# Performance work log

Measured on AMD Instinct MI355X. Metric: run time of the kernel, lower is better.

The kernel has to match this reference:

```python
import jax, jax.numpy as jnp
import numpy as np

B, L, A, D = 16, 256, 128, 4   # batch, seq_len, n_agents, per-agent feat (enc_in//n_agents)
H = 64                          # d_model / TGCN hidden
DFF = 256                       # decoder d_ff
PRED, COUT = 64, 8              # pred_len, c_out
EPS = 1e-6
SELF_W = 1.0 / EPS              # self-loop weight: 1/(0 + 1e-6)


def setup_inputs() -> dict:
    key = jax.random.key(0)
    ks = jax.random.split(key, 20)
    g = lambda i, shape, s=1.0: jax.random.normal(ks[i], shape, jnp.float32) * s
    z = lambda shape: jnp.zeros(shape, jnp.float32)
    return {
        "x": g(0, (B, L, A * D)),
        "x_mark_enc": g(1, (B, L, 4)),
        "x_dec": g(2, (B, PRED, A * D)),
        "x_mark_dec": g(3, (B, PRED, 4)),
        # GCNConv weights/biases for z, r, h gates (stored [in, out])
        "W_z": g(4, (D, H), 0.3), "b_z": z((H,)),
        "W_r": g(5, (D, H), 0.3), "b_r": z((H,)),
        "W_h": g(6, (D, H), 0.3), "b_h": z((H,)),
        # TGCN gate linears: Linear(2H, H), stored [2H, H]
        "Lz_w": g(7, (2 * H, H), 0.1), "Lz_b": z((H,)),
        "Lr_w": g(8, (2 * H, H), 0.1), "Lr_b": z((H,)),
        "Lh_w": g(9, (2 * H, H), 0.1), "Lh_b": z((H,)),
        # decoder: Linear(H, DFF) -> ReLU -> Linear(DFF, PRED*COUT)
        "D1_w": g(10, (H, DFF), 0.1), "D1_b": z((DFF,)),
        "D2_w": g(11, (DFF, PRED * COUT), 0.05), "D2_b": z((PRED * COUT,)),
    }


def _gcn(xr, a_hat, w, b):
    # GCNConv: A_hat @ (X @ W) + b, batched over (b, t)
    xw = jnp.einsum('blad,dh->blah', xr, w)
    return jnp.einsum('blae,bleh->blah', a_hat, xw) + b


def _forward(x, W_z, b_z, W_r, b_r, W_h, b_h, Lz_w, Lz_b, Lr_w, Lr_b,
             Lh_w, Lh_b, D1_w, D1_b, D2_w, D2_b):
    xr = x.reshape(B, L, A, D)
    # dense all-pairs adjacency: w_ij = 1/(||x_i-x_j|| + 1e-6); diag kept at 1e6
    sq = jnp.sum(xr * xr, axis=-1)                               # [B,L,A]
    d2 = sq[..., :, None] + sq[..., None, :] - 2.0 * jnp.einsum('blad,bled->blae', xr, xr)
    d2 = jnp.maximum(d2, 0.0)
    eye = jnp.eye(A, dtype=bool)
    dist = jnp.sqrt(jnp.where(eye, 1.0, d2))                     # safe sqrt on diag
    w = jnp.where(eye, SELF_W, 1.0 / (dist + EPS))               # [B,L,A,A]
    # symmetric GCN normalization: D^{-1/2} W D^{-1/2}
    dinv = 1.0 / jnp.sqrt(jnp.sum(w, axis=-1))                   # [B,L,A]
    a_hat = dinv[..., :, None] * w * dinv[..., None, :]
    # TGCN GRU cell with H0 = 0 (hidden state is never carried in the loop)
    cz = _gcn(xr, a_hat, W_z, b_z)
    cr = _gcn(xr, a_hat, W_r, b_r)
    ch = _gcn(xr, a_hat, W_h, b_h)
    zeros = jnp.zeros_like(cz)
    Z = jax.nn.sigmoid(jnp.concatenate([cz, zeros], -1) @ Lz_w + Lz_b)
    R = jax.nn.sigmoid(jnp.concatenate([cr, zeros], -1) @ Lr_w + Lr_b)
    Ht = jnp.tanh(jnp.concatenate([ch, zeros * R], -1) @ Lh_w + Lh_b)
    Hs = (1.0 - Z) * Ht                                          # Z*H0 + (1-Z)*Ht, H0=0
    h = jax.nn.relu(Hs)                                          # [B,L,A,H]
    pooled = h.mean(axis=2).mean(axis=1)                         # agent pool, then seq pool -> [B,H]
    y = jax.nn.relu(pooled @ D1_w + D1_b) @ D2_w + D2_b          # decoder (dropout=eval identity)
    return y.reshape(B, PRED, COUT)


def reference(x, x_mark_enc, x_dec, x_mark_dec, W_z, b_z, W_r, b_r, W_h, b_h,
              Lz_w, Lz_b, Lr_w, Lr_b, Lh_w, Lh_b, D1_w, D1_b, D2_w, D2_b):
    # x_mark_enc / x_dec / x_mark_dec are accepted but unused, as in the torch forward
    return _forward(x, W_z, b_z, W_r, b_r, W_h, b_h, Lz_w, Lz_b, Lr_w, Lr_b,
                    Lh_w, Lh_b, D1_w, D1_b, D2_w, D2_b)
```

## Files before the change

### kernel.cpp

```cpp
#include <hip/hip_runtime.h>
#include <hip/hip_bf16.h>
#include <math.h>

#define B_ 16
#define L_ 256
#define A_ 128
#define D_ 4
#define H_ 64
#define DFF_ 256
#define PRED_ 64
#define COUT_ 8

#define WS_GW   0
#define WS_GB   512
#define WS_PART 640

#define L2E 1.4426950408889634f

typedef float v2 __attribute__((ext_vector_type(2)));

__global__ __launch_bounds__(256) void precomp_kernel(
    const float* __restrict__ W_z, const float* __restrict__ b_z,
    const float* __restrict__ W_h, const float* __restrict__ b_h,
    const float* __restrict__ Lz_w, const float* __restrict__ Lz_b,
    const float* __restrict__ Lh_w, const float* __restrict__ Lh_b,
    float* __restrict__ ws)
{
    int t = threadIdx.x;
    for (int idx = t; idx < 512; idx += 256) {
        int g = idx >> 8;
        int d = (idx >> 6) & 3;
        int j = idx & 63;
        const float* W  = g ? W_h  : W_z;
        const float* Lw = g ? Lh_w : Lz_w;
        float acc = 0.f;
        for (int h = 0; h < 64; ++h)
            acc += W[d * 64 + h] * Lw[h * 64 + j];
        ws[WS_GW + g * 256 + d * 64 + j] = acc * (g ? 2.f * L2E : L2E);
    }
    if (t < 128) {
        int g = t >> 6;
        int j = t & 63;
        const float* bg = g ? b_h  : b_z;
        const float* Lw = g ? Lh_w : Lz_w;
        const float* Lb = g ? Lh_b : Lz_b;
        float acc = Lb[j];
        for (int h = 0; h < 64; ++h)
            acc += bg[h] * Lw[h * 64 + j];
        ws[WS_GB + g * 64 + j] = acc * (g ? 2.f * L2E : L2E);
    }
}

#define REP32(M) M(0) M(1) M(2) M(3) M(4) M(5) M(6) M(7) \
                 M(8) M(9) M(10) M(11) M(12) M(13) M(14) M(15) \
                 M(16) M(17) M(18) M(19) M(20) M(21) M(22) M(23) \
                 M(24) M(25) M(26) M(27) M(28) M(29) M(30) M(31)

__global__ __launch_bounds__(512, 6) void tgcn_kernel(
    const float* __restrict__ x,
    const float* __restrict__ ws_w,
    float* __restrict__ part)
{
    __shared__ float4 xr4_s[128];
    __shared__ float4 xs4_s[128];
    __shared__ float4 M4_s[128];
    __shared__ float  gw_s[512];
    __shared__ float  gb_s[128];
    __shared__ float  red_s[8][64];

    const int t  = threadIdx.x;
    const int bl = blockIdx.x;

    if (t < 128) {
        xr4_s[t] = ((const float4*)(x + (size_t)bl * (A_ * D_)))[t];
    } else if (t < 384) {
        int i = t - 128;
        gw_s[i]       = ws_w[WS_GW + i];
        gw_s[i + 256] = ws_w[WS_GW + i + 256];
    } else {
        gb_s[t - 384] = ws_w[WS_GB + (t - 384)];
    }
    __syncthreads();

    const int r = t >> 2;
    const int q = t & 3;

    const float4 xa = xr4_s[r];
    const v2 xa01 = {xa.x, xa.y};
    const v2 xa23 = {xa.z, xa.w};

#define DECLW(i) float w##i;
    REP32(DECLW)
#undef DECLW
    float rs0 = 0.f, rs1 = 0.f;
#define PASS1(i) { \
        float4 xe = xr4_s[((i) << 2) | q]; \
        v2 d01 = xa01 - (v2){xe.x, xe.y}; \
        v2 d23 = xa23 - (v2){xe.z, xe.w}; \
        v2 s2 = d01 * d01; \
        s2 = __builtin_elementwise_fma(d23, d23, s2); \
        float d2 = s2.x + s2.y; \
        w##i = fminf(__builtin_amdgcn_rsqf(d2), 1.0e6f); \
        if ((i) & 1) rs1 += w##i; else rs0 += w##i; }
    REP32(PASS1)
#undef PASS1
    float rs = rs0 + rs1;
    rs += __shfl_xor(rs, 1);
    rs += __shfl_xor(rs, 2);
    const float dinv = __builtin_amdgcn_rsqf(rs);
    if (q == 0)
        xs4_s[r] = make_float4(dinv * xa.x, dinv * xa.y, dinv * xa.z, dinv * xa.w);
    __syncthreads();

    v2 mA = {0.f, 0.f};
    v2 mB = {0.f, 0.f};
#define PASS2(i) { \
        float4 u = xs4_s[((i) << 2) | q]; \
        v2 wv2 = {w##i, w##i}; \
        mA = __builtin_elementwise_fma(wv2, (v2){u.x, u.y}, mA); \
        mB = __builtin_elementwise_fma(wv2, (v2){u.z, u.w}, mB); }
    REP32(PASS2)
#undef PASS2
    float m0 = mA.x, m1 = mA.y, m2 = mB.x, m3 = mB.y;
    m0 += __shfl_xor(m0, 1); m0 += __shfl_xor(m0, 2);
    m1 += __shfl_xor(m1, 1); m1 += __shfl_xor(m1, 2);
    m2 += __shfl_xor(m2, 1); m2 += __shfl_xor(m2, 2);
    m3 += __shfl_xor(m3, 1); m3 += __shfl_xor(m3, 2);
    if (q == 0)
        M4_s[r] = make_float4(dinv * m0, dinv * m1, dinv * m2, dinv * m3);
    __syncthreads();

    {
        const int j  = t & 63;
        const int g  = t >> 6;
        const v2 W0 = {gw_s[j],       gw_s[256 + j]};
        const v2 W1 = {gw_s[64 + j],  gw_s[320 + j]};
        const v2 W2 = {gw_s[128 + j], gw_s[384 + j]};
        const v2 W3 = {gw_s[192 + j], gw_s[448 + j]};
        const v2 Bzh = {gb_s[j], gb_s[64 + j]};
        float acc = 0.f;
        #pragma unroll
        for (int i = 0; i < 16; ++i) {
            float4 mv = M4_s[g * 16 + i];
            v2 zh = __builtin_elementwise_fma((v2){mv.x, mv.x}, W0, Bzh);
            zh = __builtin_elementwise_fma((v2){mv.y, mv.y}, W1, zh);
            zh = __builtin_elementwise_fma((v2){mv.z, mv.z}, W2, zh);
            zh = __builtin_elementwise_fma((v2){mv.w, mv.w}, W3, zh);
            float ez = __builtin_amdgcn_exp2f(zh.x);
            float e2 = __builtin_amdgcn_exp2f(zh.y);
            float num = e2 - 1.f;
            float den = (1.f + ez) * (1.f + e2);
            float hv  = num * __builtin_amdgcn_rcpf(den);
            acc += fmaxf(hv, 0.f);
        }
        red_s[g][j] = acc;
    }
    __syncthreads();

    if (t < 64) {
        float s = red_s[0][t] + red_s[1][t] + red_s[2][t] + red_s[3][t]
                + red_s[4][t] + red_s[5][t] + red_s[6][t] + red_s[7][t];
        part[(size_t)bl * 64 + t] = s;
    }
}

__global__ __launch_bounds__(1024) void pooldec_kernel(
    const float* __restrict__ part,
    const float* __restrict__ D1_w, const float* __restrict__ D1_b,
    const float* __restrict__ D2_w, const float* __restrict__ D2_b,
    float* __restrict__ out)
{
    __shared__ float red_s[16][64];
    __shared__ float pooled_s[64];
    __shared__ float t1_s[256];
    const int t = threadIdx.x, b = blockIdx.x;

    {
        const int j = t & 63, g = t >> 6;
        const float* pb = part + ((size_t)b * L_ + g * 16) * 64;
        float s = 0.f;
        #pragma unroll
        for (int i = 0; i < 16; ++i) s += pb[i * 64 + j];
        red_s[g][j] = s;
    }
    __syncthreads();
    if (t < 64) {
        float s = 0.f;
        #pragma unroll
        for (int g = 0; g < 16; ++g) s += red_s[g][t];
        pooled_s[t] = s * (1.f / ((float)L_ * (float)A_));
    }
    __syncthreads();

    {
        const int o = t >> 2, sub = t & 3;
        float acc = 0.f;
        #pragma unroll
        for (int hh = 0; hh < 16; ++hh) {
            int h = sub * 16 + hh;
            acc += pooled_s[h] * D1_w[h * 256 + o];
        }
        acc += __shfl_xor(acc, 1);
        acc += __shfl_xor(acc, 2);
        if (sub == 0) t1_s[o] = fmaxf(acc + D1_b[o], 0.f);
    }
    __syncthreads();

    {
        const int o = t >> 1, kh = t & 1;
        float acc = 0.f;
        for (int kk = 0; kk < 128; ++kk) {
            int k = kh * 128 + kk;
            acc += t1_s[k] * D2_w[k * 512 + o];
        }
        acc += __shfl_xor(acc, 1);
        if (kh == 0) out[(size_t)b * 512 + o] = acc + D2_b[o];
    }
}

extern "C" void kernel_launch(void* const* d_in, const int* in_sizes, int n_in,
                              void* d_out, int out_size, void* d_ws, size_t ws_size,
                              hipStream_t stream)
{
    const float* x    = (const float*)d_in[0];
    const float* W_z  = (const float*)d_in[4];
    const float* b_z  = (const float*)d_in[5];
    const float* W_h  = (const float*)d_in[8];
    const float* b_h  = (const float*)d_in[9];
    const float* Lz_w = (const float*)d_in[10];
    const float* Lz_b = (const float*)d_in[11];
    const float* Lh_w = (const float*)d_in[14];
    const float* Lh_b = (const float*)d_in[15];
    const float* D1_w = (const float*)d_in[16];
    const float* D1_b = (const float*)d_in[17];
    const float* D2_w = (const float*)d_in[18];
    const float* D2_b = (const float*)d_in[19];

    float* ws  = (float*)d_ws;
    float* out = (float*)d_out;

    precomp_kernel<<<1, 256, 0, stream>>>(W_z, b_z, W_h, b_h,
                                          Lz_w, Lz_b, Lh_w, Lh_b, ws);
    tgcn_kernel<<<B_ * L_, 512, 0, stream>>>(x, ws, ws + WS_PART);
    pooldec_kernel<<<B_, 1024, 0, stream>>>(ws + WS_PART, D1_w, D1_b,
                                            D2_w, D2_b, out);
}
```

Measured before the change: 69.73 us.

## Process two agent rows per thread in TGCN kernel with 256-thread blocks

Halves the block size of the main TGCN kernel and has each thread compute adjacency weights and aggregation for two agent rows (r and r+64). Each neighbour float4 loaded from shared memory is reused for both rows, which cuts LDS traffic per FLOP, and the gate stage loops over 32 agents per group instead of 16. The trade-off is double the register arrays for the weights (64 floats) and lower thread-level parallelism per block, which may reduce occupancy or add spills.

```diff
diff --git a/kernel.cpp b/kernel.cpp
--- a/kernel.cpp
+++ b/kernel.cpp
@@ -51,12 +51,7 @@
     }
 }
 
-#define REP32(M) M(0) M(1) M(2) M(3) M(4) M(5) M(6) M(7) \
-                 M(8) M(9) M(10) M(11) M(12) M(13) M(14) M(15) \
-                 M(16) M(17) M(18) M(19) M(20) M(21) M(22) M(23) \
-                 M(24) M(25) M(26) M(27) M(28) M(29) M(30) M(31)
-
-__global__ __launch_bounds__(512, 6) void tgcn_kernel(
+__global__ __launch_bounds__(256, 4) void tgcn_kernel(
     const float* __restrict__ x,
     const float* __restrict__ ws_w,
     float* __restrict__ part)
@@ -66,68 +61,99 @@
     __shared__ float4 M4_s[128];
     __shared__ float  gw_s[512];
     __shared__ float  gb_s[128];
-    __shared__ float  red_s[8][64];
+    __shared__ float  red_s[4][64];
 
     const int t  = threadIdx.x;
     const int bl = blockIdx.x;
 
     if (t < 128) {
         xr4_s[t] = ((const float4*)(x + (size_t)bl * (A_ * D_)))[t];
-    } else if (t < 384) {
-        int i = t - 128;
-        gw_s[i]       = ws_w[WS_GW + i];
-        gw_s[i + 256] = ws_w[WS_GW + i + 256];
-    } else {
-        gb_s[t - 384] = ws_w[WS_GB + (t - 384)];
-    }
+        gb_s[t]  = ws_w[WS_GB + t];
+    }
+    gw_s[t]       = ws_w[WS_GW + t];
+    gw_s[t + 256] = ws_w[WS_GW + t + 256];
     __syncthreads();
 
     const int r = t >> 2;
     const int q = t & 3;
 
-    const float4 xa = xr4_s[r];
-    const v2 xa01 = {xa.x, xa.y};
-    const v2 xa23 = {xa.z, xa.w};
-
-#define DECLW(i) float w##i;
-    REP32(DECLW)
-#undef DECLW
-    float rs0 = 0.f, rs1 = 0.f;
-#define PASS1(i) { \
-        float4 xe = xr4_s[((i) << 2) | q]; \
-        v2 d01 = xa01 - (v2){xe.x, xe.y}; \
-        v2 d23 = xa23 - (v2){xe.z, xe.w}; \
-        v2 s2 = d01 * d01; \
-        s2 = __builtin_elementwise_fma(d23, d23, s2); \
-        float d2 = s2.x + s2.y; \
-        w##i = fminf(__builtin_amdgcn_rsqf(d2), 1.0e6f); \
-        if ((i) & 1) rs1 += w##i; else rs0 += w##i; }
-    REP32(PASS1)
-#undef PASS1
-    float rs = rs0 + rs1;
-    rs += __shfl_xor(rs, 1);
-    rs += __shfl_xor(rs, 2);
-    const float dinv = __builtin_amdgcn_rsqf(rs);
-    if (q == 0)
-        xs4_s[r] = make_float4(dinv * xa.x, dinv * xa.y, dinv * xa.z, dinv * xa.w);
-    __syncthreads();
-
-    v2 mA = {0.f, 0.f};
-    v2 mB = {0.f, 0.f};
-#define PASS2(i) { \
-        float4 u = xs4_s[((i) << 2) | q]; \
-        v2 wv2 = {w##i, w##i}; \
-        mA = __builtin_elementwise_fma(wv2, (v2){u.x, u.y}, mA); \
-        mB = __builtin_elementwise_fma(wv2, (v2){u.z, u.w}, mB); }
-    REP32(PASS2)
-#undef PASS2
-    float m0 = mA.x, m1 = mA.y, m2 = mB.x, m3 = mB.y;
-    m0 += __shfl_xor(m0, 1); m0 += __shfl_xor(m0, 2);
-    m1 += __shfl_xor(m1, 1); m1 += __shfl_xor(m1, 2);
-    m2 += __shfl_xor(m2, 1); m2 += __shfl_xor(m2, 2);
-    m3 += __shfl_xor(m3, 1); m3 += __shfl_xor(m3, 2);
-    if (q == 0)
-        M4_s[r] = make_float4(dinv * m0, dinv * m1, dinv * m2, dinv * m3);
+    const float4 xa0 = xr4_s[r];
+    const float4 xa1 = xr4_s[r + 64];
+    const v2 a0_01 = {xa0.x, xa0.y};
+    const v2 a0_23 = {xa0.z, xa0.w};
+    const v2 a1_01 = {xa1.x, xa1.y};
+    const v2 a1_23 = {xa1.z, xa1.w};
+
+    float wu[32];
+    float wv[32];
+    float rsA0 = 0.f, rsA1 = 0.f, rsB0 = 0.f, rsB1 = 0.f;
+    #pragma unroll
+    for (int k = 0; k < 32; ++k) {
+        float4 xe = xr4_s[(k << 2) | q];
+        v2 e01 = {xe.x, xe.y};
+        v2 e23 = {xe.z, xe.w};
+        v2 dA01 = a0_01 - e01;
+        v2 dA23 = a0_23 - e23;
+        v2 sA = dA01 * dA01;
+        sA = __builtin_elementwise_fma(dA23, dA23, sA);
+        float wA = fminf(__builtin_amdgcn_rsqf(sA.x + sA.y), 1.0e6f);
+        v2 dB01 = a1_01 - e01;
+        v2 dB23 = a1_23 - e23;
+        v2 sB = dB01 * dB01;
+        sB = __builtin_elementwise_fma(dB23, dB23, sB);
+        float wB = fminf(__builtin_amdgcn_rsqf(sB.x + sB.y), 1.0e6f);
+        wu[k] = wA;
+        wv[k] = wB;
+        if (k & 1) { rsA1 += wA; rsB1 += wB; }
+        else       { rsA0 += wA; rsB0 += wB; }
+    }
+    float rsA = rsA0 + rsA1;
+    float rsB = rsB0 + rsB1;
+    rsA += __shfl_xor(rsA, 1); rsA += __shfl_xor(rsA, 2);
+    rsB += __shfl_xor(rsB, 1); rsB += __shfl_xor(rsB, 2);
+    const float dinvA = __builtin_amdgcn_rsqf(rsA);
+    const float dinvB = __builtin_amdgcn_rsqf(rsB);
+    if (q == 0) {
+        xs4_s[r]      = make_float4(dinvA * xa0.x, dinvA * xa0.y,
+                                    dinvA * xa0.z, dinvA * xa0.w);
+        xs4_s[r + 64] = make_float4(dinvB * xa1.x, dinvB * xa1.y,
+                                    dinvB * xa1.z, dinvB * xa1.w);
+    }
+    __syncthreads();
+
+    v2 mA01 = {0.f, 0.f};
+    v2 mA23 = {0.f, 0.f};
+    v2 mB01 = {0.f, 0.f};
+    v2 mB23 = {0.f, 0.f};
+    #pragma unroll
+    for (int k = 0; k < 32; ++k) {
+        float4 xu = xr4_s[0];
+        xu = xs4_s[(k << 2) | q];
+        v2 u01 = {xu.x, xu.y};
+        v2 u23 = {xu.z, xu.w};
+        v2 wA2 = {wu[k], wu[k]};
+        v2 wB2 = {wv[k], wv[k]};
+        mA01 = __builtin_elementwise_fma(wA2, u01, mA01);
+        mA23 = __builtin_elementwise_fma(wA2, u23, mA23);
+        mB01 = __builtin_elementwise_fma(wB2, u01, mB01);
+        mB23 = __builtin_elementwise_fma(wB2, u23, mB23);
+    }
+    float mA0 = mA01.x, mA1 = mA01.y, mA2 = mA23.x, mA3 = mA23.y;
+    float mB0 = mB01.x, mB1 = mB01.y, mB2 = mB23.x, mB3 = mB23.y;
+    mA0 += __shfl_xor(mA0, 1); mA0 += __shfl_xor(mA0, 2);
+    mA1 += __shfl_xor(mA1, 1); mA1 += __shfl_xor(mA1, 2);
+    mA2 += __shfl_xor(mA2, 1); mA2 += __shfl_xor(mA2, 2);
+    mA3 += __shfl_xor(mA3, 1); mA3 += __shfl_xor(mA3, 2);
+    mB0 += __shfl_xor(mB0, 1); mB0 += __shfl_xor(mB0, 2);
+    mB1 += __shfl_xor(mB1, 1); mB1 += __shfl_xor(mB1, 2);
+    mB2 += __shfl_xor(mB2, 1); mB2 += __shfl_xor(mB2, 2);
+    mB3 += __shfl_xor(mB3, 1); mB3 += __shfl_xor(mB3, 2);
+    if (q == 0) {
+        M4_s[r]      = make_float4(dinvA * mA0, dinvA * mA1,
+                                   dinvA * mA2, dinvA * mA3);
+        M4_s[r + 64] = make_float4(dinvB * mB0, dinvB * mB1,
+                                   dinvB * mB2, dinvB * mB3);
+    }
     __syncthreads();
 
     {
@@ -140,8 +166,8 @@
         const v2 Bzh = {gb_s[j], gb_s[64 + j]};
         float acc = 0.f;
         #pragma unroll
-        for (int i = 0; i < 16; ++i) {
-            float4 mv = M4_s[g * 16 + i];
+        for (int i = 0; i < 32; ++i) {
+            float4 mv = M4_s[g * 32 + i];
             v2 zh = __builtin_elementwise_fma((v2){mv.x, mv.x}, W0, Bzh);
             zh = __builtin_elementwise_fma((v2){mv.y, mv.y}, W1, zh);
             zh = __builtin_elementwise_fma((v2){mv.z, mv.z}, W2, zh);
@@ -158,9 +184,8 @@
     __syncthreads();
 
     if (t < 64) {
-        float s = red_s[0][t] + red_s[1][t] + red_s[2][t] + red_s[3][t]
-                + red_s[4][t] + red_s[5][t] + red_s[6][t] + red_s[7][t];
-        part[(size_t)bl * 64 + t] = s;
+        part[(size_t)bl * 64 + t] = red_s[0][t] + red_s[1][t]
+                                  + red_s[2][t] + red_s[3][t];
     }
 }
 
@@ -241,7 +266,7 @@
 
     precomp_kernel<<<1, 256, 0, stream>>>(W_z, b_z, W_h, b_h,
                                           Lz_w, Lz_b, Lh_w, Lh_b, ws);
-    tgcn_kernel<<<B_ * L_, 512, 0, stream>>>(x, ws, ws + WS_PART);
+    tgcn_kernel<<<B_ * L_, 256, 0, stream>>>(x, ws, ws + WS_PART);
     pooldec_kernel<<<B_, 1024, 0, stream>>>(ws + WS_PART, D1_w, D1_b,
                                             D2_w, D2_b, out);
 }
```

Result: slower. 79.93 us (+14.6%).

## Recompute adjacency weights instead of caching, two rows per thread group

Applied to the files above, without the earlier changes.

The TGCN kernel no longer holds 32 adjacency weights per thread in registers. Each 8-thread group now handles two agent rows and recomputes the distance-based weights in the aggregation pass, folding the neighbour's dinv in directly, so the scaled-x shared buffer becomes a per-agent dinv array. This trades roughly double the rsqrt and distance arithmetic for lower register pressure and shared reuse of each neighbour load across two rows, and the occupancy hint drops from 6 to 4. The tiny weight-precompute kernel is also spread over 5 blocks with partial unrolling.

```diff
diff --git a/kernel.cpp b/kernel.cpp
--- a/kernel.cpp
+++ b/kernel.cpp
@@ -19,50 +19,47 @@
 
 typedef float v2 __attribute__((ext_vector_type(2)));
 
-__global__ __launch_bounds__(256) void precomp_kernel(
+__global__ __launch_bounds__(128) void precomp_kernel(
     const float* __restrict__ W_z, const float* __restrict__ b_z,
     const float* __restrict__ W_h, const float* __restrict__ b_h,
     const float* __restrict__ Lz_w, const float* __restrict__ Lz_b,
     const float* __restrict__ Lh_w, const float* __restrict__ Lh_b,
     float* __restrict__ ws)
 {
-    int t = threadIdx.x;
-    for (int idx = t; idx < 512; idx += 256) {
-        int g = idx >> 8;
-        int d = (idx >> 6) & 3;
-        int j = idx & 63;
+    const int idx = blockIdx.x * 128 + threadIdx.x;
+    if (idx < 512) {
+        const int g = idx >> 8;
+        const int d = (idx >> 6) & 3;
+        const int j = idx & 63;
         const float* W  = g ? W_h  : W_z;
         const float* Lw = g ? Lh_w : Lz_w;
         float acc = 0.f;
+        #pragma unroll 8
         for (int h = 0; h < 64; ++h)
             acc += W[d * 64 + h] * Lw[h * 64 + j];
         ws[WS_GW + g * 256 + d * 64 + j] = acc * (g ? 2.f * L2E : L2E);
-    }
-    if (t < 128) {
-        int g = t >> 6;
-        int j = t & 63;
+    } else {
+        const int i = idx - 512;
+        const int g = i >> 6;
+        const int j = i & 63;
         const float* bg = g ? b_h  : b_z;
         const float* Lw = g ? Lh_w : Lz_w;
         const float* Lb = g ? Lh_b : Lz_b;
         float acc = Lb[j];
+        #pragma unroll 8
         for (int h = 0; h < 64; ++h)
             acc += bg[h] * Lw[h * 64 + j];
         ws[WS_GB + g * 64 + j] = acc * (g ? 2.f * L2E : L2E);
     }
 }
 
-#define REP32(M) M(0) M(1) M(2) M(3) M(4) M(5) M(6) M(7) \
-                 M(8) M(9) M(10) M(11) M(12) M(13) M(14) M(15) \
-                 M(16) M(17) M(18) M(19) M(20) M(21) M(22) M(23) \
-                 M(24) M(25) M(26) M(27) M(28) M(29) M(30) M(31)
-
-__global__ __launch_bounds__(512, 6) void tgcn_kernel(
+__global__ __launch_bounds__(512, 4) void tgcn_kernel(
     const float* __restrict__ x,
     const float* __restrict__ ws_w,
     float* __restrict__ part)
 {
     __shared__ float4 xr4_s[128];
-    __shared__ float4 xs4_s[128];
+    __shared__ float  dinv_s[128];
     __shared__ float4 M4_s[128];
     __shared__ float  gw_s[512];
     __shared__ float  gb_s[128];
@@ -71,68 +68,80 @@
     const int t  = threadIdx.x;
     const int bl = blockIdx.x;
 
-    if (t < 128) {
+    if (t < 128)
         xr4_s[t] = ((const float4*)(x + (size_t)bl * (A_ * D_)))[t];
-    } else if (t < 384) {
-        int i = t - 128;
-        gw_s[i]       = ws_w[WS_GW + i];
-        gw_s[i + 256] = ws_w[WS_GW + i + 256];
-    } else {
-        gb_s[t - 384] = ws_w[WS_GB + (t - 384)];
-    }
-    __syncthreads();
-
-    const int r = t >> 2;
-    const int q = t & 3;
-
-    const float4 xa = xr4_s[r];
-    const v2 xa01 = {xa.x, xa.y};
-    const v2 xa23 = {xa.z, xa.w};
-
-#define DECLW(i) float w##i;
-    REP32(DECLW)
-#undef DECLW
-    float rs0 = 0.f, rs1 = 0.f;
-#define PASS1(i) { \
-        float4 xe = xr4_s[((i) << 2) | q]; \
-        v2 d01 = xa01 - (v2){xe.x, xe.y}; \
-        v2 d23 = xa23 - (v2){xe.z, xe.w}; \
-        v2 s2 = d01 * d01; \
-        s2 = __builtin_elementwise_fma(d23, d23, s2); \
-        float d2 = s2.x + s2.y; \
-        w##i = fminf(__builtin_amdgcn_rsqf(d2), 1.0e6f); \
-        if ((i) & 1) rs1 += w##i; else rs0 += w##i; }
-    REP32(PASS1)
-#undef PASS1
-    float rs = rs0 + rs1;
-    rs += __shfl_xor(rs, 1);
-    rs += __shfl_xor(rs, 2);
-    const float dinv = __builtin_amdgcn_rsqf(rs);
-    if (q == 0)
-        xs4_s[r] = make_float4(dinv * xa.x, dinv * xa.y, dinv * xa.z, dinv * xa.w);
-    __syncthreads();
-
-    v2 mA = {0.f, 0.f};
-    v2 mB = {0.f, 0.f};
-#define PASS2(i) { \
-        float4 u = xs4_s[((i) << 2) | q]; \
-        v2 wv2 = {w##i, w##i}; \
-        mA = __builtin_elementwise_fma(wv2, (v2){u.x, u.y}, mA); \
-        mB = __builtin_elementwise_fma(wv2, (v2){u.z, u.w}, mB); }
-    REP32(PASS2)
-#undef PASS2
-    float m0 = mA.x, m1 = mA.y, m2 = mB.x, m3 = mB.y;
-    m0 += __shfl_xor(m0, 1); m0 += __shfl_xor(m0, 2);
-    m1 += __shfl_xor(m1, 1); m1 += __shfl_xor(m1, 2);
-    m2 += __shfl_xor(m2, 1); m2 += __shfl_xor(m2, 2);
-    m3 += __shfl_xor(m3, 1); m3 += __shfl_xor(m3, 2);
-    if (q == 0)
-        M4_s[r] = make_float4(dinv * m0, dinv * m1, dinv * m2, dinv * m3);
-    __syncthreads();
-
-    {
-        const int j  = t & 63;
-        const int g  = t >> 6;
+    gw_s[t] = ws_w[WS_GW + t];
+    if (t < 128) gb_s[t] = ws_w[WS_GB + t];
+    __syncthreads();
+
+    const int r = t >> 3;
+    const int q = t & 7;
+
+    const float4 xa0 = xr4_s[r];
+    const float4 xa1 = xr4_s[r + 64];
+
+    float rsA = 0.f, rsB = 0.f;
+    #pragma unroll
+    for (int k = 0; k < 16; ++k) {
+        float4 xe = xr4_s[(k << 3) | q];
+        float ax = xa0.x - xe.x, ay = xa0.y - xe.y;
+        float az = xa0.z - xe.z, aw = xa0.w - xe.w;
+        float dA = ax * ax + ay * ay + az * az + aw * aw;
+        rsA += fminf(__builtin_amdgcn_rsqf(dA), 1.0e6f);
+        float bx = xa1.x - xe.x, by = xa1.y - xe.y;
+        float bz = xa1.z - xe.z, bw = xa1.w - xe.w;
+        float dB = bx * bx + by * by + bz * bz + bw * bw;
+        rsB += fminf(__builtin_amdgcn_rsqf(dB), 1.0e6f);
+    }
+    rsA += __shfl_xor(rsA, 1); rsA += __shfl_xor(rsA, 2); rsA += __shfl_xor(rsA, 4);
+    rsB += __shfl_xor(rsB, 1); rsB += __shfl_xor(rsB, 2); rsB += __shfl_xor(rsB, 4);
+    const float dinvA = __builtin_amdgcn_rsqf(rsA);
+    const float dinvB = __builtin_amdgcn_rsqf(rsB);
+    if (q == 0) {
+        dinv_s[r]      = dinvA;
+        dinv_s[r + 64] = dinvB;
+    }
+    __syncthreads();
+
+    float mA0 = 0.f, mA1 = 0.f, mA2 = 0.f, mA3 = 0.f;
+    float mB0 = 0.f, mB1 = 0.f, mB2 = 0.f, mB3 = 0.f;
+    #pragma unroll
+    for (int k = 0; k < 16; ++k) {
+        const int e = (k << 3) | q;
+        float4 xe = xr4_s[e];
+        float de = dinv_s[e];
+        float ax = xa0.x - xe.x, ay = xa0.y - xe.y;
+        float az = xa0.z - xe.z, aw = xa0.w - xe.w;
+        float dA = ax * ax + ay * ay + az * az + aw * aw;
+        float wA = fminf(__builtin_amdgcn_rsqf(dA), 1.0e6f) * de;
+        float bx = xa1.x - xe.x, by = xa1.y - xe.y;
+        float bz = xa1.z - xe.z, bw = xa1.w - xe.w;
+        float dB = bx * bx + by * by + bz * bz + bw * bw;
+        float wB = fminf(__builtin_amdgcn_rsqf(dB), 1.0e6f) * de;
+        mA0 = fmaf(wA, xe.x, mA0); mA1 = fmaf(wA, xe.y, mA1);
+        mA2 = fmaf(wA, xe.z, mA2); mA3 = fmaf(wA, xe.w, mA3);
+        mB0 = fmaf(wB, xe.x, mB0); mB1 = fmaf(wB, xe.y, mB1);
+        mB2 = fmaf(wB, xe.z, mB2); mB3 = fmaf(wB, xe.w, mB3);
+    }
+    mA0 += __shfl_xor(mA0, 1); mA0 += __shfl_xor(mA0, 2); mA0 += __shfl_xor(mA0, 4);
+    mA1 += __shfl_xor(mA1, 1); mA1 += __shfl_xor(mA1, 2); mA1 += __shfl_xor(mA1, 4);
+    mA2 += __shfl_xor(mA2, 1); mA2 += __shfl_xor(mA2, 2); mA2 += __shfl_xor(mA2, 4);
+    mA3 += __shfl_xor(mA3, 1); mA3 += __shfl_xor(mA3, 2); mA3 += __shfl_xor(mA3, 4);
+    mB0 += __shfl_xor(mB0, 1); mB0 += __shfl_xor(mB0, 2); mB0 += __shfl_xor(mB0, 4);
+    mB1 += __shfl_xor(mB1, 1); mB1 += __shfl_xor(mB1, 2); mB1 += __shfl_xor(mB1, 4);
+    mB2 += __shfl_xor(mB2, 1); mB2 += __shfl_xor(mB2, 2); mB2 += __shfl_xor(mB2, 4);
+    mB3 += __shfl_xor(mB3, 1); mB3 += __shfl_xor(mB3, 2); mB3 += __shfl_xor(mB3, 4);
+    if (q == 0) {
+        M4_s[r]      = make_float4(dinvA * mA0, dinvA * mA1,
+                                   dinvA * mA2, dinvA * mA3);
+        M4_s[r + 64] = make_float4(dinvB * mB0, dinvB * mB1,
+                                   dinvB * mB2, dinvB * mB3);
+    }
+    __syncthreads();
+
+    {
+        const int j = t & 63;
+        const int g = t >> 6;
         const v2 W0 = {gw_s[j],       gw_s[256 + j]};
         const v2 W1 = {gw_s[64 + j],  gw_s[320 + j]};
         const v2 W2 = {gw_s[128 + j], gw_s[384 + j]};
@@ -239,7 +248,7 @@
     float* ws  = (float*)d_ws;
     float* out = (float*)d_out;
 
-    precomp_kernel<<<1, 256, 0, stream>>>(W_z, b_z, W_h, b_h,
+    precomp_kernel<<<5, 128, 0, stream>>>(W_z, b_z, W_h, b_h,
                                           Lz_w, Lz_b, Lh_w, Lh_b, ws);
     tgcn_kernel<<<B_ * L_, 512, 0, stream>>>(x, ws, ws + WS_PART);
     pooldec_kernel<<<B_, 1024, 0, stream>>>(ws + WS_PART, D1_w, D1_b,
```

After: 88.81 us. 27.4% more time.
